# Kernel tuning notes

Measured on AMD Instinct MI355X. Metric: run time of the kernel, lower is better.

## Reference

```python
import jax, jax.numpy as jnp
import numpy as np
from jax.ops import segment_sum

N_PFAS, N_GW, N_SW = 50000, 200000, 20000
D_IN, D_OUT, D_EDGE = 32, 32, 3
E_PG, E_GP, E_PS, E_SP = 2000000, 2000000, 1000000, 1000000


def _params(key):
    ks = jax.random.split(key, 24)
    g = lambda k, s: jax.random.normal(k, s, dtype=jnp.float32) * 0.05
    p = {}
    # SAGEConvWithEdgeAttr for pg (pfas->gw) and gp (gw->pfas)
    for i, rel in enumerate(['pg', 'gp']):
        o = i * 5
        p[f'Wl_{rel}'] = g(ks[o + 0], (D_IN, D_OUT))
        p[f'bl_{rel}'] = g(ks[o + 1], (D_OUT,))
        p[f'Wr_{rel}'] = g(ks[o + 2], (D_IN, D_OUT))
        p[f'We_{rel}'] = g(ks[o + 3], (D_EDGE, D_OUT))
        p[f'be_{rel}'] = g(ks[o + 4], (D_OUT,))
    # plain SAGEConv for ps (pfas->sw) and sp (sw->pfas)
    for i, rel in enumerate(['ps', 'sp']):
        o = 10 + i * 3
        p[f'Wl_{rel}'] = g(ks[o + 0], (D_IN, D_OUT))
        p[f'bl_{rel}'] = g(ks[o + 1], (D_OUT,))
        p[f'Wr_{rel}'] = g(ks[o + 2], (D_IN, D_OUT))
    p['W_out'] = g(ks[16], (D_OUT, 1))
    p['b_out'] = g(ks[17], (1,))
    p['a_prelu'] = jnp.float32(0.25) * jnp.ones((1,), jnp.float32)
    return p


def setup_inputs() -> dict:
    key = jax.random.key(0)
    ks = jax.random.split(key, 16)
    inp = {
        'x_pfas': jax.random.normal(ks[0], (N_PFAS, D_IN), jnp.float32),
        'x_gw': jax.random.normal(ks[1], (N_GW, D_IN), jnp.float32),
        'x_sw': jax.random.normal(ks[2], (N_SW, D_IN), jnp.float32),
        'src_pg': jax.random.randint(ks[3], (E_PG,), 0, N_PFAS),
        'dst_pg': jax.random.randint(ks[4], (E_PG,), 0, N_GW),
        'ea_pg': jax.random.uniform(ks[5], (E_PG, D_EDGE), jnp.float32),
        'src_gp': jax.random.randint(ks[6], (E_GP,), 0, N_GW),
        'dst_gp': jax.random.randint(ks[7], (E_GP,), 0, N_PFAS),
        'ea_gp': jax.random.uniform(ks[8], (E_GP, D_EDGE), jnp.float32),
        'src_ps': jax.random.randint(ks[9], (E_PS,), 0, N_PFAS),
        'dst_ps': jax.random.randint(ks[10], (E_PS,), 0, N_SW),
        'src_sp': jax.random.randint(ks[11], (E_SP,), 0, N_SW),
        'dst_sp': jax.random.randint(ks[12], (E_SP,), 0, N_PFAS),
    }
    inp.update(_params(ks[13]))
    return inp


def _sage(x_src, x_dst, src, dst, Wl, bl, Wr, n_dst):
    # PyG SAGEConv: lin_l(mean_aggr(x_j)) + lin_r(x_dst); lin_r has no bias
    msg = x_src[src]                                   # [E, D_IN]
    s = segment_sum(msg, dst, num_segments=n_dst)      # [n_dst, D_IN]
    cnt = segment_sum(jnp.ones((src.shape[0],), x_src.dtype), dst, num_segments=n_dst)
    mean = s / jnp.maximum(cnt, 1.0)[:, None]
    return mean @ Wl + bl + x_dst @ Wr


def _edge_scatter_set(dst, ea_t, n_dst):
    # matches torch zeros.scatter_(0, col, edge_attr_transformed): overwrite at dst
    return jnp.zeros((n_dst, ea_t.shape[1]), ea_t.dtype).at[dst].set(ea_t)


def reference(x_pfas, x_gw, x_sw,
              src_pg, dst_pg, ea_pg,
              src_gp, dst_gp, ea_gp,
              src_ps, dst_ps, src_sp, dst_sp,
              Wl_pg, bl_pg, Wr_pg, We_pg, be_pg,
              Wl_gp, bl_gp, Wr_gp, We_gp, be_gp,
              Wl_ps, bl_ps, Wr_ps,
              Wl_sp, bl_sp, Wr_sp,
              W_out, b_out, a_prelu):
    # pfas -> gw (edge attrs)
    out_gw = _sage(x_pfas, x_gw, src_pg, dst_pg, Wl_pg, bl_pg, Wr_pg, N_GW)
    out_gw = out_gw + _edge_scatter_set(dst_pg, ea_pg @ We_pg + be_pg, N_GW)
    # gw -> pfas (edge attrs)
    out_pf1 = _sage(x_gw, x_pfas, src_gp, dst_gp, Wl_gp, bl_gp, Wr_gp, N_PFAS)
    out_pf1 = out_pf1 + _edge_scatter_set(dst_gp, ea_gp @ We_gp + be_gp, N_PFAS)
    # sw -> pfas (plain SAGE)
    out_pf2 = _sage(x_sw, x_pfas, src_sp, dst_sp, Wl_sp, bl_sp, Wr_sp, N_PFAS)
    # pfas -> sw (plain SAGE)
    out_sw = _sage(x_pfas, x_sw, src_ps, dst_ps, Wl_ps, bl_ps, Wr_ps, N_SW)
    # HeteroConv aggr='sum' over relations with same dst type, then relu
    h_pfas = jax.nn.relu(out_pf1 + out_pf2)
    h_gw = jax.nn.relu(out_gw)
    h_sw = jax.nn.relu(out_sw)
    # final linear + PReLU on gw_wells
    y = h_gw @ W_out + b_out                           # [N_GW, 1]
    y = jnp.where(y >= 0, y, a_prelu * y)
    return h_pfas, y, h_sw
```

## Files before the change

kernel.cpp:

```cpp
#include <hip/hip_runtime.h>
#include <hip/hip_fp16.h>

typedef unsigned int u32;
typedef unsigned long long u64;

#define NPFAS 50000
#define NGW   200000
#define NSW   20000
#define D     32
#define EPG   2000000
#define EGP   2000000
#define EPS   1000000
#define ESP   1000000

#define NB_PG 782
#define NB_GP 782
#define NB_SP 391
#define NB_PS 313
#define CAP_PG 2880
#define CAP_GP 2880
#define CAP_SP 2880
#define CAP_PS 3584
#define SORT_MAX 3584

#define ZGCUR    0
#define MAXE_PG  2304
#define MAXE_GP  202304
#define S_PG     252304
#define S_GP     6652304
#define S_SP     8252304
#define S_PS     9852304
#define CNT_PG   10492304
#define CNT_GP   10692304
#define CNT_SP   10742304
#define CNT_PS   10792304
#define REG_PG   10812304
#define REG_GP   15316624
#define REG_SP   19820944
#define REG_PS   20947024
#define XH_PFAS  22068816
#define XH_GW    22868816

#define PART_BLOCKS 512
#define CONV_BLOCKS 256

__device__ __forceinline__ void part4_narrow(
    const int* __restrict__ src, const int* __restrict__ dst,
    int e0, int e1, int nb, int cp, int cf, int pshift, int bbits, int roundSz,
    u32* __restrict__ region, int cap, int* __restrict__ gcur,
    u32* binData, u32* binCnt)
{
    u32 dlm = (1u << bbits) - 1u;
    for (int b = threadIdx.x; b < nb; b += 256) binCnt[b] = 0;
    __syncthreads();
    for (int base = e0; base < e1; base += roundSz) {
        int rend = base + roundSz; if (rend > e1) rend = e1;
        for (int e = base + (int)threadIdx.x; e < rend; e += 256) {
            int d = dst[e];
            int bk = d >> bbits;
            u32 w0 = (u32)src[e] | (((u32)d & dlm) << pshift);
            u32 pos = atomicAdd(&binCnt[bk], 1u);
            if ((int)pos < cp) {
                binData[bk * cp + (int)pos] = w0;
            } else {
                int g = atomicAdd(&gcur[bk], 1);
                if (g < cap) region[(size_t)bk * cap + g] = w0;
            }
        }
        __syncthreads();
        bool last = (base + roundSz >= e1);
        for (int b = threadIdx.x; b < nb; b += 256) {
            int c = (int)binCnt[b];
            if (c > cp) c = cp;
            if (c >= cf || (last && c > 0)) {
                int g = atomicAdd(&gcur[b], c);
                int lim = cap - g; if (lim < 0) lim = 0; if (c > lim) c = lim;
                u32* dp = region + ((size_t)b * cap + g);
                for (int i = 0; i < c; i++) dp[i] = binData[b * cp + i];
                binCnt[b] = 0;
            }
        }
        __syncthreads();
    }
}

__device__ __forceinline__ void part4_wide(
    const int* __restrict__ src, const int* __restrict__ dst,
    int e0, int e1, int nb, int cp, int cf, int bbits, int roundSz,
    u64* __restrict__ region, int cap, int* __restrict__ gcur,
    u64* binData, u32* binCnt)
{
    u32 dlm = (1u << bbits) - 1u;
    for (int b = threadIdx.x; b < nb; b += 256) binCnt[b] = 0;
    __syncthreads();
    for (int base = e0; base < e1; base += roundSz) {
        int rend = base + roundSz; if (rend > e1) rend = e1;
        for (int e = base + (int)threadIdx.x; e < rend; e += 256) {
            int d = dst[e];
            int bk = d >> bbits;
            u64 w0 = ((u64)(u32)e << 32) | (u32)src[e] | (((u32)d & dlm) << 21);
            u32 pos = atomicAdd(&binCnt[bk], 1u);
            if ((int)pos < cp) {
                binData[bk * cp + (int)pos] = w0;
            } else {
                int g = atomicAdd(&gcur[bk], 1);
                if (g < cap) region[(size_t)bk * cap + g] = w0;
            }
        }
        __syncthreads();
        bool last = (base + roundSz >= e1);
        for (int b = threadIdx.x; b < nb; b += 256) {
            int c = (int)binCnt[b];
            if (c > cp) c = cp;
            if (c >= cf || (last && c > 0)) {
                int g = atomicAdd(&gcur[b], c);
                int lim = cap - g; if (lim < 0) lim = 0; if (c > lim) c = lim;
                u64* dp = region + ((size_t)b * cap + g);
                for (int i = 0; i < c; i++) dp[i] = binData[b * cp + i];
                binCnt[b] = 0;
            }
        }
        __syncthreads();
    }
}

__global__ __launch_bounds__(256) void partition_conv(
    const int* __restrict__ src_pg, const int* __restrict__ dst_pg,
    const int* __restrict__ src_gp, const int* __restrict__ dst_gp,
    const int* __restrict__ src_sp, const int* __restrict__ dst_sp,
    const int* __restrict__ src_ps, const int* __restrict__ dst_ps,
    const float* __restrict__ x_pfas, const float* __restrict__ x_gw,
    int* __restrict__ wsi)
{
    __shared__ __align__(16) u64 binData64[6256];
    __shared__ u32 binCnt[782];
    u32* ws = (u32*)wsi;
    int b = blockIdx.x;
    if (b >= PART_BLOCKS) {
        __half2* hp = (__half2*)(wsi + XH_PFAS);
        __half2* hg = (__half2*)(wsi + XH_GW);
        const float2* fp = (const float2*)x_pfas;
        const float2* fg = (const float2*)x_gw;
        int idx = (b - PART_BLOCKS) * 256 + (int)threadIdx.x;
        const int NTP = NPFAS * D / 2;
        const int NTT = NTP + NGW * D / 2;
        for (int i = idx; i < NTT; i += CONV_BLOCKS * 256) {
            if (i < NTP) {
                float2 v = fp[i];
                hp[i] = __floats2half2_rn(v.x, v.y);
            } else {
                float2 v = fg[i - NTP];
                hg[i - NTP] = __floats2half2_rn(v.x, v.y);
            }
        }
        return;
    }
    if (b < 160) {
        int e0 = b * (EPG / 160);
        part4_wide(src_pg, dst_pg, e0, e0 + EPG / 160, NB_PG, 8, 6, 8, 2048,
                   (u64*)(ws + REG_PG), CAP_PG, wsi + ZGCUR + 0, binData64, binCnt);
    } else if (b < 320) {
        int bb = b - 160;
        int e0 = bb * (EGP / 160);
        part4_wide(src_gp, dst_gp, e0, e0 + EGP / 160, NB_GP, 8, 6, 6, 2048,
                   (u64*)(ws + REG_GP), CAP_GP, wsi + ZGCUR + 782, binData64, binCnt);
    } else if (b < 416) {
        int bb = b - 320;
        int e0 = (int)(((long long)bb * ESP) / 96);
        int e1 = (int)(((long long)(bb + 1) * ESP) / 96);
        part4_narrow(src_sp, dst_sp, e0, e1, NB_SP, 32, 24, 15, 7, 2048,
                     ws + REG_SP, CAP_SP, wsi + ZGCUR + 1564, (u32*)binData64, binCnt);
    } else {
        int bb = b - 416;
        int e0 = (int)(((long long)bb * EPS) / 96);
        int e1 = (int)(((long long)(bb + 1) * EPS) / 96);
        part4_narrow(src_ps, dst_ps, e0, e1, NB_PS, 32, 24, 16, 6, 2048,
                     ws + REG_PS, CAP_PS, wsi + ZGCUR + 1955, (u32*)binData64, binCnt);
    }
}

__global__ __launch_bounds__(256) void sort_agg(
    const float* __restrict__ x_sw,
    int* __restrict__ wsi)
{
    __shared__ u32 sortedS[SORT_MAX];
    __shared__ int histS[256];
    __shared__ int startS[256];
    __shared__ int cursorS[256];
    __shared__ int mxS[256];
    __shared__ int wsum[4];

    float* wsf = (float*)wsi;
    u32* wsu = (u32*)wsi;
    int tid = threadIdx.x;
    int bid = blockIdx.x;

    const __half2* xh2 = nullptr; const float2* xf2 = nullptr;
    const u64* reg64 = nullptr; const u32* reg32 = nullptr;
    int gi, cap, pshift, nbDst, dbase, ndst;
    u32 smask; bool wide; float* sOut; float* cntOut; int* mxOut = nullptr;

    if (bid < NB_PG) {
        xh2 = (const __half2*)(wsi + XH_PFAS);
        reg64 = (const u64*)(wsu + REG_PG) + (size_t)bid * CAP_PG; gi = ZGCUR + bid;
        cap = CAP_PG; pshift = 21; smask = 0x1FFFFFu; wide = true;
        nbDst = 256; dbase = bid << 8; ndst = NGW;
        sOut = wsf + S_PG; cntOut = wsf + CNT_PG; mxOut = wsi + MAXE_PG;
    } else if (bid < NB_PG + NB_GP) {
        int b = bid - NB_PG;
        xh2 = (const __half2*)(wsi + XH_GW);
        reg64 = (const u64*)(wsu + REG_GP) + (size_t)b * CAP_GP; gi = ZGCUR + 782 + b;
        cap = CAP_GP; pshift = 21; smask = 0x1FFFFFu; wide = true;
        nbDst = 64; dbase = b << 6; ndst = NPFAS;
        sOut = wsf + S_GP; cntOut = wsf + CNT_GP; mxOut = wsi + MAXE_GP;
    } else if (bid < NB_PG + NB_GP + NB_SP) {
        int b = bid - NB_PG - NB_GP;
        xf2 = (const float2*)x_sw;
        reg32 = wsu + REG_SP + (size_t)b * CAP_SP; gi = ZGCUR + 1564 + b;
        cap = CAP_SP; pshift = 15; smask = 0x7FFFu; wide = false;
        nbDst = 128; dbase = b << 7; ndst = NPFAS;
        sOut = wsf + S_SP; cntOut = wsf + CNT_SP;
    } else {
        int b = bid - NB_PG - NB_GP - NB_SP;
        xh2 = (const __half2*)(wsi + XH_PFAS);
        reg32 = wsu + REG_PS + (size_t)b * CAP_PS; gi = ZGCUR + 1955 + b;
        cap = CAP_PS; pshift = 16; smask = 0xFFFFu; wide = false;
        nbDst = 64; dbase = b << 6; ndst = NSW;
        sOut = wsf + S_PS; cntOut = wsf + CNT_PS;
    }

    int nEnt = wsi[gi]; if (nEnt > cap) nEnt = cap;

    histS[tid] = 0;
    mxS[tid] = -1;
    __syncthreads();

    if (wide) {
        for (int i = tid; i < nEnt; i += 256) {
            u64 w = reg64[i];
            int dl = (int)(((u32)w >> 21) & 255u);
            atomicAdd(&histS[dl], 1);
            atomicMax(&mxS[dl], (int)(u32)(w >> 32));
        }
    } else {
        for (int i = tid; i < nEnt; i += 256) {
            u32 w = reg32[i];
            int dl = (int)((w >> pshift) & 255u);
            atomicAdd(&histS[dl], 1);
        }
    }
    __syncthreads();

    {
        int v = histS[tid];
        int lane = tid & 63, w = tid >> 6;
        int incl = v;
#pragma unroll
        for (int off = 1; off < 64; off <<= 1) {
            int t = __shfl_up(incl, off);
            if (lane >= off) incl += t;
        }
        if (lane == 63) wsum[w] = incl;
        startS[tid] = incl - v;
    }
    __syncthreads();
    {
        int w = tid >> 6;
        int off = 0;
        for (int k = 0; k < w; k++) off += wsum[k];
        int st = startS[tid] + off;
        startS[tid] = st;
        cursorS[tid] = st;
    }
    __syncthreads();

    if (wide) {
        for (int i = tid; i < nEnt; i += 256) {
            u64 w = reg64[i];
            int dl = (int)(((u32)w >> 21) & 255u);
            int pos = atomicAdd(&cursorS[dl], 1);
            if (pos < SORT_MAX) sortedS[pos] = (u32)w & smask;
        }
    } else {
        for (int i = tid; i < nEnt; i += 256) {
            u32 w = reg32[i];
            int dl = (int)((w >> pshift) & 255u);
            int pos = atomicAdd(&cursorS[dl], 1);
            if (pos < SORT_MAX) sortedS[pos] = w & smask;
        }
    }
    __syncthreads();

    int wv = tid >> 6, lane = tid & 63;
    int rs = lane >> 4;
    int fp = lane & 15;
    for (int q = wv; q < nbDst; q += 4) {
        int dn = dbase + q;
        if (dn >= ndst) continue;
        int deg = histS[q];
        int p0 = startS[q];
        float ax = 0.f, ay = 0.f;
        int i = 0;
        if (xh2) {
            for (; i + 7 < deg; i += 8) {
                int s0 = (int)sortedS[p0 + i + rs];
                int s1 = (int)sortedS[p0 + i + 4 + rs];
                __half2 h0 = xh2[s0 * 16 + fp];
                __half2 h1 = xh2[s1 * 16 + fp];
                float2 f0 = __half22float2(h0);
                float2 f1 = __half22float2(h1);
                ax += f0.x + f1.x;
                ay += f0.y + f1.y;
            }
            for (; i < deg; i += 4) {
                if (i + rs < deg) {
                    int s0 = (int)sortedS[p0 + i + rs];
                    float2 f0 = __half22float2(xh2[s0 * 16 + fp]);
                    ax += f0.x; ay += f0.y;
                }
            }
        } else {
            for (; i + 7 < deg; i += 8) {
                int s0 = (int)sortedS[p0 + i + rs];
                int s1 = (int)sortedS[p0 + i + 4 + rs];
                float2 f0 = xf2[s0 * 16 + fp];
                float2 f1 = xf2[s1 * 16 + fp];
                ax += f0.x + f1.x;
                ay += f0.y + f1.y;
            }
            for (; i < deg; i += 4) {
                if (i + rs < deg) {
                    int s0 = (int)sortedS[p0 + i + rs];
                    float2 f0 = xf2[s0 * 16 + fp];
                    ax += f0.x; ay += f0.y;
                }
            }
        }
        ax += __shfl_xor(ax, 16); ay += __shfl_xor(ay, 16);
        ax += __shfl_xor(ax, 32); ay += __shfl_xor(ay, 32);
        if (rs == 0) {
            float2* so2 = (float2*)(sOut + (size_t)dn * D);
            so2[fp] = make_float2(ax, ay);
        }
        if (lane == 0) {
            cntOut[dn] = (float)deg;
            if (wide) mxOut[dn] = mxS[q];
        }
    }
}

#define GW_B   782
#define PFAS_B 196
#define SW_B   79

__global__ __launch_bounds__(256) void finalize_all(
    const float* __restrict__ s_pg, const float* __restrict__ cnt_pg,
    const int* __restrict__ maxe_pg, const float* __restrict__ x_gw,
    const float* __restrict__ ea_pg,
    const float* __restrict__ Wl_pg, const float* __restrict__ bl_pg,
    const float* __restrict__ Wr_pg, const float* __restrict__ We_pg,
    const float* __restrict__ be_pg,
    const float* __restrict__ W_out, const float* __restrict__ b_out,
    const float* __restrict__ a_prelu,
    const float* __restrict__ s_gp, const float* __restrict__ cnt_gp,
    const int* __restrict__ maxe_gp,
    const float* __restrict__ s_sp, const float* __restrict__ cnt_sp,
    const float* __restrict__ x_pfas, const float* __restrict__ ea_gp,
    const float* __restrict__ Wl_gp, const float* __restrict__ bl_gp,
    const float* __restrict__ Wr_gp, const float* __restrict__ We_gp,
    const float* __restrict__ be_gp,
    const float* __restrict__ Wl_sp, const float* __restrict__ bl_sp,
    const float* __restrict__ Wr_sp,
    const float* __restrict__ s_ps, const float* __restrict__ cnt_ps,
    const float* __restrict__ x_sw,
    const float* __restrict__ Wl_ps, const float* __restrict__ bl_ps,
    const float* __restrict__ Wr_ps,
    float* __restrict__ h_pfas, float* __restrict__ y_out, float* __restrict__ h_sw)
{
    __shared__ __align__(16) float sh[3328];
    int tid = threadIdx.x;
    int b = blockIdx.x;

    if (b < GW_B) {
        float* WlT = sh;
        float* WrT = sh + 1024;
        float* WeT = sh + 2048;
        float* blS = sh + 2144;
        float* beS = sh + 2176;
        float* WoS = sh + 2208;
        for (int i = tid; i < D * D; i += 256) {
            int k = i / D, j = i % D;
            WlT[j * D + k] = Wl_pg[i];
            WrT[j * D + k] = Wr_pg[i];
        }
        for (int i = tid; i < 3 * D; i += 256) {
            int k = i / D, j = i % D;
            WeT[j * 3 + k] = We_pg[i];
        }
        if (tid < D) {
            blS[tid] = bl_pg[tid];
            beS[tid] = be_pg[tid];
            WoS[tid] = W_out[tid];
        }
        __syncthreads();

        int n = b * 256 + tid;
        if (n >= NGW) return;

        float mean[D], xd[D];
        float inv = 1.0f / fmaxf(cnt_pg[n], 1.0f);
        const float4* sp = (const float4*)(s_pg + (size_t)n * D);
        const float4* xp = (const float4*)(x_gw + (size_t)n * D);
#pragma unroll
        for (int q = 0; q < D / 4; q++) {
            float4 sv = sp[q];
            mean[4*q+0] = sv.x * inv; mean[4*q+1] = sv.y * inv;
            mean[4*q+2] = sv.z * inv; mean[4*q+3] = sv.w * inv;
            float4 xv = xp[q];
            xd[4*q+0] = xv.x; xd[4*q+1] = xv.y; xd[4*q+2] = xv.z; xd[4*q+3] = xv.w;
        }
        int me = maxe_pg[n];
        bool he = (me >= 0);
        float e0 = 0.f, e1 = 0.f, e2 = 0.f;
        if (he) {
            e0 = ea_pg[(size_t)me * 3 + 0];
            e1 = ea_pg[(size_t)me * 3 + 1];
            e2 = ea_pg[(size_t)me * 3 + 2];
        }
        float yacc = 0.f;
        for (int j = 0; j < D; j++) {
            float o = blS[j] + (he ? beS[j] : 0.0f);
            const float4* wl4 = (const float4*)(WlT + j * D);
            const float4* wr4 = (const float4*)(WrT + j * D);
#pragma unroll
            for (int q = 0; q < D / 4; q++) {
                float4 wl = wl4[q], wr = wr4[q];
                o += mean[4*q+0]*wl.x + mean[4*q+1]*wl.y + mean[4*q+2]*wl.z + mean[4*q+3]*wl.w;
                o += xd[4*q+0]*wr.x + xd[4*q+1]*wr.y + xd[4*q+2]*wr.z + xd[4*q+3]*wr.w;
            }
            if (he) o += e0*WeT[j*3+0] + e1*WeT[j*3+1] + e2*WeT[j*3+2];
            float h = fmaxf(o, 0.0f);
            yacc += h * WoS[j];
        }
        float y = yacc + b_out[0];
        float ap = a_prelu[0];
        y_out[n] = (y >= 0.f) ? y : ap * y;

    } else if (b < GW_B + PFAS_B) {
        float* WlgT = sh;
        float* WlsT = sh + 1024;
        float* WrcT = sh + 2048;
        float* WeT  = sh + 3072;
        float* blc  = sh + 3168;
        float* beS  = sh + 3200;
        for (int i = tid; i < D * D; i += 256) {
            int k = i / D, j = i % D;
            WlgT[j * D + k] = Wl_gp[i];
            WlsT[j * D + k] = Wl_sp[i];
            WrcT[j * D + k] = Wr_gp[i] + Wr_sp[i];
        }
        for (int i = tid; i < 3 * D; i += 256) {
            int k = i / D, j = i % D;
            WeT[j * 3 + k] = We_gp[i];
        }
        if (tid < D) {
            blc[tid] = bl_gp[tid] + bl_sp[tid];
            beS[tid] = be_gp[tid];
        }
        __syncthreads();

        int n = (b - GW_B) * 256 + tid;
        if (n >= NPFAS) return;

        float mg[D], ms[D], xd[D];
        float invg = 1.0f / fmaxf(cnt_gp[n], 1.0f);
        float invs = 1.0f / fmaxf(cnt_sp[n], 1.0f);
        const float4* gp4 = (const float4*)(s_gp + (size_t)n * D);
        const float4* sp4 = (const float4*)(s_sp + (size_t)n * D);
        const float4* xp4 = (const float4*)(x_pfas + (size_t)n * D);
#pragma unroll
        for (int q = 0; q < D / 4; q++) {
            float4 a = gp4[q];
            mg[4*q+0] = a.x * invg; mg[4*q+1] = a.y * invg; mg[4*q+2] = a.z * invg; mg[4*q+3] = a.w * invg;
            float4 bb = sp4[q];
            ms[4*q+0] = bb.x * invs; ms[4*q+1] = bb.y * invs; ms[4*q+2] = bb.z * invs; ms[4*q+3] = bb.w * invs;
            float4 c = xp4[q];
            xd[4*q+0] = c.x; xd[4*q+1] = c.y; xd[4*q+2] = c.z; xd[4*q+3] = c.w;
        }
        int me = maxe_gp[n];
        bool he = (me >= 0);
        float e0 = 0.f, e1 = 0.f, e2 = 0.f;
        if (he) {
            e0 = ea_gp[(size_t)me * 3 + 0];
            e1 = ea_gp[(size_t)me * 3 + 1];
            e2 = ea_gp[(size_t)me * 3 + 2];
        }
        float* out = h_pfas + (size_t)n * D;
        for (int j = 0; j < D; j++) {
            float o = blc[j] + (he ? beS[j] : 0.0f);
            const float4* wg4 = (const float4*)(WlgT + j * D);
            const float4* ws4 = (const float4*)(WlsT + j * D);
            const float4* wc4 = (const float4*)(WrcT + j * D);
#pragma unroll
            for (int q = 0; q < D / 4; q++) {
                float4 wg = wg4[q], wsv = ws4[q], wc = wc4[q];
                o += mg[4*q+0]*wg.x + mg[4*q+1]*wg.y + mg[4*q+2]*wg.z + mg[4*q+3]*wg.w;
                o += ms[4*q+0]*wsv.x + ms[4*q+1]*wsv.y + ms[4*q+2]*wsv.z + ms[4*q+3]*wsv.w;
                o += xd[4*q+0]*wc.x + xd[4*q+1]*wc.y + xd[4*q+2]*wc.z + xd[4*q+3]*wc.w;
            }
            if (he) o += e0*WeT[j*3+0] + e1*WeT[j*3+1] + e2*WeT[j*3+2];
            out[j] = fmaxf(o, 0.0f);
        }

    } else {
        float* WlT = sh;
        float* WrT = sh + 1024;
        float* blS = sh + 2048;
        for (int i = tid; i < D * D; i += 256) {
            int k = i / D, j = i % D;
            WlT[j * D + k] = Wl_ps[i];
            WrT[j * D + k] = Wr_ps[i];
        }
        if (tid < D) blS[tid] = bl_ps[tid];
        __syncthreads();

        int n = (b - GW_B - PFAS_B) * 256 + tid;
        if (n >= NSW) return;

        float mean[D], xd[D];
        float inv = 1.0f / fmaxf(cnt_ps[n], 1.0f);
        const float4* sp = (const float4*)(s_ps + (size_t)n * D);
        const float4* xp = (const float4*)(x_sw + (size_t)n * D);
#pragma unroll
        for (int q = 0; q < D / 4; q++) {
            float4 sv = sp[q];
            mean[4*q+0] = sv.x * inv; mean[4*q+1] = sv.y * inv;
            mean[4*q+2] = sv.z * inv; mean[4*q+3] = sv.w * inv;
            float4 xv = xp[q];
            xd[4*q+0] = xv.x; xd[4*q+1] = xv.y; xd[4*q+2] = xv.z; xd[4*q+3] = xv.w;
        }
        float* out = h_sw + (size_t)n * D;
        for (int j = 0; j < D; j++) {
            float o = blS[j];
            const float4* wl4 = (const float4*)(WlT + j * D);
            const float4* wr4 = (const float4*)(WrT + j * D);
#pragma unroll
            for (int q = 0; q < D / 4; q++) {
                float4 wl = wl4[q], wr = wr4[q];
                o += mean[4*q+0]*wl.x + mean[4*q+1]*wl.y + mean[4*q+2]*wl.z + mean[4*q+3]*wl.w;
                o += xd[4*q+0]*wr.x + xd[4*q+1]*wr.y + xd[4*q+2]*wr.z + xd[4*q+3]*wr.w;
            }
            out[j] = fmaxf(o, 0.0f);
        }
    }
}

extern "C" void kernel_launch(void* const* d_in, const int* in_sizes, int n_in,
                              void* d_out, int out_size, void* d_ws, size_t ws_size,
                              hipStream_t stream) {
    (void)in_sizes; (void)n_in; (void)out_size; (void)ws_size;
    const float* x_pfas = (const float*)d_in[0];
    const float* x_gw   = (const float*)d_in[1];
    const float* x_sw   = (const float*)d_in[2];
    const int*   src_pg = (const int*)d_in[3];
    const int*   dst_pg = (const int*)d_in[4];
    const float* ea_pg  = (const float*)d_in[5];
    const int*   src_gp = (const int*)d_in[6];
    const int*   dst_gp = (const int*)d_in[7];
    const float* ea_gp  = (const float*)d_in[8];
    const int*   src_ps = (const int*)d_in[9];
    const int*   dst_ps = (const int*)d_in[10];
    const int*   src_sp = (const int*)d_in[11];
    const int*   dst_sp = (const int*)d_in[12];
    const float* Wl_pg = (const float*)d_in[13];
    const float* bl_pg = (const float*)d_in[14];
    const float* Wr_pg = (const float*)d_in[15];
    const float* We_pg = (const float*)d_in[16];
    const float* be_pg = (const float*)d_in[17];
    const float* Wl_gp = (const float*)d_in[18];
    const float* bl_gp = (const float*)d_in[19];
    const float* Wr_gp = (const float*)d_in[20];
    const float* We_gp = (const float*)d_in[21];
    const float* be_gp = (const float*)d_in[22];
    const float* Wl_ps = (const float*)d_in[23];
    const float* bl_ps = (const float*)d_in[24];
    const float* Wr_ps = (const float*)d_in[25];
    const float* Wl_sp = (const float*)d_in[26];
    const float* bl_sp = (const float*)d_in[27];
    const float* Wr_sp = (const float*)d_in[28];
    const float* W_out = (const float*)d_in[29];
    const float* b_out = (const float*)d_in[30];
    const float* a_pre = (const float*)d_in[31];

    int*   wsi = (int*)d_ws;
    float* wsf = (float*)d_ws;

    hipMemsetAsync(wsi + ZGCUR, 0, 2304 * sizeof(int), stream);

    partition_conv<<<PART_BLOCKS + CONV_BLOCKS, 256, 0, stream>>>(
        src_pg, dst_pg, src_gp, dst_gp,
        src_sp, dst_sp, src_ps, dst_ps,
        x_pfas, x_gw, wsi);

    sort_agg<<<NB_PG + NB_GP + NB_SP + NB_PS, 256, 0, stream>>>(x_sw, wsi);

    float* out    = (float*)d_out;
    float* h_pfas = out;
    float* y_out  = out + 1600000;
    float* h_sw   = out + 1800000;

    finalize_all<<<GW_B + PFAS_B + SW_B, 256, 0, stream>>>(
        wsf + S_PG, wsf + CNT_PG, wsi + MAXE_PG, x_gw, ea_pg,
        Wl_pg, bl_pg, Wr_pg, We_pg, be_pg, W_out, b_out, a_pre,
        wsf + S_GP, wsf + CNT_GP, wsi + MAXE_GP, wsf + S_SP, wsf + CNT_SP,
        x_pfas, ea_gp,
        Wl_gp, bl_gp, Wr_gp, We_gp, be_gp,
        Wl_sp, bl_sp, Wr_sp,
        wsf + S_PS, wsf + CNT_PS, x_sw, Wl_ps, bl_ps, Wr_ps,
        h_pfas, y_out, h_sw);
}
```

Measured before the change: 436.2 us.

## Replace shared-memory bin buffering with two-pass count-then-scatter partitioning

Swaps the per-block shared-memory staging bins, with their periodic flushes to global buckets, for a two-pass scheme. Each block first histograms its edges into buckets, reserves contiguous global ranges with one atomic per bucket, then rereads the edges and scatters them straight to their slots. Block counts per relation also rise (256/256/128/128), and the smaller shared footprint should allow more resident blocks. In exchange the dst array is read twice and the global writes are scattered rather than written as buffered runs.

```diff
diff --git a/kernel.cpp b/kernel.cpp
--- a/kernel.cpp
+++ b/kernel.cpp
@@ -41,86 +41,64 @@
 #define XH_PFAS  22068816
 #define XH_GW    22868816
 
-#define PART_BLOCKS 512
+#define PB_PG 256
+#define PB_GP 256
+#define PB_SP 128
+#define PB_PS 128
+#define PART_BLOCKS (PB_PG + PB_GP + PB_SP + PB_PS)
 #define CONV_BLOCKS 256
 
-__device__ __forceinline__ void part4_narrow(
+__device__ __forceinline__ void part2_wide(
     const int* __restrict__ src, const int* __restrict__ dst,
-    int e0, int e1, int nb, int cp, int cf, int pshift, int bbits, int roundSz,
+    int e0, int e1, int nb, int bbits,
+    u64* __restrict__ region, int cap, int* __restrict__ gcur,
+    int* cntS)
+{
+    int tid = threadIdx.x;
+    u32 dlm = (1u << bbits) - 1u;
+    for (int i = tid; i < nb; i += 256) cntS[i] = 0;
+    __syncthreads();
+    for (int e = e0 + tid; e < e1; e += 256)
+        atomicAdd(&cntS[dst[e] >> bbits], 1);
+    __syncthreads();
+    for (int i = tid; i < nb; i += 256) {
+        int c = cntS[i];
+        cntS[i] = (c > 0) ? atomicAdd(&gcur[i], c) : 0;
+    }
+    __syncthreads();
+    for (int e = e0 + tid; e < e1; e += 256) {
+        int d = dst[e];
+        int bk = d >> bbits;
+        u64 w0 = ((u64)(u32)e << 32) | (u32)src[e] | (((u32)d & dlm) << 21);
+        int slot = atomicAdd(&cntS[bk], 1);
+        if (slot < cap) region[(size_t)bk * cap + slot] = w0;
+    }
+}
+
+__device__ __forceinline__ void part2_narrow(
+    const int* __restrict__ src, const int* __restrict__ dst,
+    int e0, int e1, int nb, int bbits, int pshift,
     u32* __restrict__ region, int cap, int* __restrict__ gcur,
-    u32* binData, u32* binCnt)
+    int* cntS)
 {
+    int tid = threadIdx.x;
     u32 dlm = (1u << bbits) - 1u;
-    for (int b = threadIdx.x; b < nb; b += 256) binCnt[b] = 0;
-    __syncthreads();
-    for (int base = e0; base < e1; base += roundSz) {
-        int rend = base + roundSz; if (rend > e1) rend = e1;
-        for (int e = base + (int)threadIdx.x; e < rend; e += 256) {
-            int d = dst[e];
-            int bk = d >> bbits;
-            u32 w0 = (u32)src[e] | (((u32)d & dlm) << pshift);
-            u32 pos = atomicAdd(&binCnt[bk], 1u);
-            if ((int)pos < cp) {
-                binData[bk * cp + (int)pos] = w0;
-            } else {
-                int g = atomicAdd(&gcur[bk], 1);
-                if (g < cap) region[(size_t)bk * cap + g] = w0;
-            }
-        }
-        __syncthreads();
-        bool last = (base + roundSz >= e1);
-        for (int b = threadIdx.x; b < nb; b += 256) {
-            int c = (int)binCnt[b];
-            if (c > cp) c = cp;
-            if (c >= cf || (last && c > 0)) {
-                int g = atomicAdd(&gcur[b], c);
-                int lim = cap - g; if (lim < 0) lim = 0; if (c > lim) c = lim;
-                u32* dp = region + ((size_t)b * cap + g);
-                for (int i = 0; i < c; i++) dp[i] = binData[b * cp + i];
-                binCnt[b] = 0;
-            }
-        }
-        __syncthreads();
-    }
-}
-
-__device__ __forceinline__ void part4_wide(
-    const int* __restrict__ src, const int* __restrict__ dst,
-    int e0, int e1, int nb, int cp, int cf, int bbits, int roundSz,
-    u64* __restrict__ region, int cap, int* __restrict__ gcur,
-    u64* binData, u32* binCnt)
-{
-    u32 dlm = (1u << bbits) - 1u;
-    for (int b = threadIdx.x; b < nb; b += 256) binCnt[b] = 0;
-    __syncthreads();
-    for (int base = e0; base < e1; base += roundSz) {
-        int rend = base + roundSz; if (rend > e1) rend = e1;
-        for (int e = base + (int)threadIdx.x; e < rend; e += 256) {
-            int d = dst[e];
-            int bk = d >> bbits;
-            u64 w0 = ((u64)(u32)e << 32) | (u32)src[e] | (((u32)d & dlm) << 21);
-            u32 pos = atomicAdd(&binCnt[bk], 1u);
-            if ((int)pos < cp) {
-                binData[bk * cp + (int)pos] = w0;
-            } else {
-                int g = atomicAdd(&gcur[bk], 1);
-                if (g < cap) region[(size_t)bk * cap + g] = w0;
-            }
-        }
-        __syncthreads();
-        bool last = (base + roundSz >= e1);
-        for (int b = threadIdx.x; b < nb; b += 256) {
-            int c = (int)binCnt[b];
-            if (c > cp) c = cp;
-            if (c >= cf || (last && c > 0)) {
-                int g = atomicAdd(&gcur[b], c);
-                int lim = cap - g; if (lim < 0) lim = 0; if (c > lim) c = lim;
-                u64* dp = region + ((size_t)b * cap + g);
-                for (int i = 0; i < c; i++) dp[i] = binData[b * cp + i];
-                binCnt[b] = 0;
-            }
-        }
-        __syncthreads();
+    for (int i = tid; i < nb; i += 256) cntS[i] = 0;
+    __syncthreads();
+    for (int e = e0 + tid; e < e1; e += 256)
+        atomicAdd(&cntS[dst[e] >> bbits], 1);
+    __syncthreads();
+    for (int i = tid; i < nb; i += 256) {
+        int c = cntS[i];
+        cntS[i] = (c > 0) ? atomicAdd(&gcur[i], c) : 0;
+    }
+    __syncthreads();
+    for (int e = e0 + tid; e < e1; e += 256) {
+        int d = dst[e];
+        int bk = d >> bbits;
+        u32 w0 = (u32)src[e] | (((u32)d & dlm) << pshift);
+        int slot = atomicAdd(&cntS[bk], 1);
+        if (slot < cap) region[(size_t)bk * cap + slot] = w0;
     }
 }
 
@@ -132,8 +110,7 @@
     const float* __restrict__ x_pfas, const float* __restrict__ x_gw,
     int* __restrict__ wsi)
 {
-    __shared__ __align__(16) u64 binData64[6256];
-    __shared__ u32 binCnt[782];
+    __shared__ int cntS[NB_PG];
     u32* ws = (u32*)wsi;
     int b = blockIdx.x;
     if (b >= PART_BLOCKS) {
@@ -155,27 +132,29 @@
         }
         return;
     }
-    if (b < 160) {
-        int e0 = b * (EPG / 160);
-        part4_wide(src_pg, dst_pg, e0, e0 + EPG / 160, NB_PG, 8, 6, 8, 2048,
-                   (u64*)(ws + REG_PG), CAP_PG, wsi + ZGCUR + 0, binData64, binCnt);
-    } else if (b < 320) {
-        int bb = b - 160;
-        int e0 = bb * (EGP / 160);
-        part4_wide(src_gp, dst_gp, e0, e0 + EGP / 160, NB_GP, 8, 6, 6, 2048,
-                   (u64*)(ws + REG_GP), CAP_GP, wsi + ZGCUR + 782, binData64, binCnt);
-    } else if (b < 416) {
-        int bb = b - 320;
-        int e0 = (int)(((long long)bb * ESP) / 96);
-        int e1 = (int)(((long long)(bb + 1) * ESP) / 96);
-        part4_narrow(src_sp, dst_sp, e0, e1, NB_SP, 32, 24, 15, 7, 2048,
-                     ws + REG_SP, CAP_SP, wsi + ZGCUR + 1564, (u32*)binData64, binCnt);
+    if (b < PB_PG) {
+        int e0 = (int)(((long long)b * EPG) / PB_PG);
+        int e1 = (int)(((long long)(b + 1) * EPG) / PB_PG);
+        part2_wide(src_pg, dst_pg, e0, e1, NB_PG, 8,
+                   (u64*)(ws + REG_PG), CAP_PG, wsi + ZGCUR + 0, cntS);
+    } else if (b < PB_PG + PB_GP) {
+        int bb = b - PB_PG;
+        int e0 = (int)(((long long)bb * EGP) / PB_GP);
+        int e1 = (int)(((long long)(bb + 1) * EGP) / PB_GP);
+        part2_wide(src_gp, dst_gp, e0, e1, NB_GP, 6,
+                   (u64*)(ws + REG_GP), CAP_GP, wsi + ZGCUR + 782, cntS);
+    } else if (b < PB_PG + PB_GP + PB_SP) {
+        int bb = b - PB_PG - PB_GP;
+        int e0 = (int)(((long long)bb * ESP) / PB_SP);
+        int e1 = (int)(((long long)(bb + 1) * ESP) / PB_SP);
+        part2_narrow(src_sp, dst_sp, e0, e1, NB_SP, 7, 15,
+                     ws + REG_SP, CAP_SP, wsi + ZGCUR + 1564, cntS);
     } else {
-        int bb = b - 416;
-        int e0 = (int)(((long long)bb * EPS) / 96);
-        int e1 = (int)(((long long)(bb + 1) * EPS) / 96);
-        part4_narrow(src_ps, dst_ps, e0, e1, NB_PS, 32, 24, 16, 6, 2048,
-                     ws + REG_PS, CAP_PS, wsi + ZGCUR + 1955, (u32*)binData64, binCnt);
+        int bb = b - PB_PG - PB_GP - PB_SP;
+        int e0 = (int)(((long long)bb * EPS) / PB_PS);
+        int e1 = (int)(((long long)(bb + 1) * EPS) / PB_PS);
+        part2_narrow(src_ps, dst_ps, e0, e1, NB_PS, 6, 16,
+                     ws + REG_PS, CAP_PS, wsi + ZGCUR + 1955, cntS);
     }
 }
 
```

Measured after the change: 473.2 us. 8.5% more time.
